# Optimization experiments

Measured on AMD Instinct MI355X. Metric: run time of the kernel, lower is better.

Reference implementation:

```python
import jax, jax.numpy as jnp
import numpy as np


def setup_inputs() -> dict:
    key = jax.random.key(0)
    k1, k2 = jax.random.split(key)
    support_features = jax.random.normal(k1, (1000, 5, 512), dtype=jnp.float32)
    query_features = jax.random.normal(k2, (5000, 512), dtype=jnp.float32)
    return {"support_features": support_features, "query_features": query_features, "use_cosine": 1}


def reference(support_features, query_features, use_cosine):
    # Preprocess: mean-center over (classes, shots), then L2-normalize per vector.
    mean = jnp.mean(support_features, axis=(0, 1), keepdims=True)  # [1,1,D]
    s = support_features - mean                                    # [C,S,D]
    q = query_features - mean[0]                                   # [Q,D]
    s = s / jnp.linalg.norm(s, axis=2, keepdims=True)
    q = q / jnp.linalg.norm(q, axis=1, keepdims=True)
    if use_cosine:
        # cosine sims without materializing [C,Q,S,D]; einsum fuses the dot.
        sims = jnp.einsum('csd,qd->cqs', s, q)   # [C,Q,S]
        best = jnp.max(sims, axis=2)             # [C,Q] best shot per class
        return jnp.argmax(best, axis=0)          # [Q] predicted class
    else:
        # euclidean cdist(query[Q,D], support[C,S,D]) -> [C,Q,S]
        d2 = (jnp.sum(q * q, axis=1)[None, :, None]
              + jnp.sum(s * s, axis=2)[:, None, :]
              - 2.0 * jnp.einsum('csd,qd->cqs', s, q))
        dist = jnp.sqrt(jnp.maximum(d2, 0.0))
        best = jnp.min(dist, axis=2)
        return jnp.argmin(best, axis=0)
```

## Files before the change

kernel.cpp:

```cpp
#include <hip/hip_runtime.h>
#include <stdint.h>

#define D     512
#define NSUP  5000
#define NQRY  5000
#define NPAD  5120
#define MEAN_BLOCKS 100
#define ROWS_PER_MEAN_BLOCK 50
#define SCALE 512.0f

#define OFF_SHI     0
#define OFF_SLO     5242880
#define OFF_QHI     10485760
#define OFF_QLO     15728640
#define OFF_PARTIAL 20971520
#define OFF_MEAN    21176320
#define OFF_KEYS    21178368

typedef _Float16 half4v __attribute__((ext_vector_type(4)));
typedef _Float16 half8v __attribute__((ext_vector_type(8)));
typedef float    f32x4  __attribute__((ext_vector_type(4)));

__device__ __forceinline__ unsigned long long pack_key(float v, int sidx) {
    unsigned u = __float_as_uint(v);
    u = (u & 0x80000000u) ? ~u : (u | 0x80000000u);
    return ((unsigned long long)u << 32) | (unsigned)(0xFFFFFFFFu - (unsigned)sidx);
}

__device__ __forceinline__ void gload16(const void* g, void* l) {
    __builtin_amdgcn_global_load_lds(
        (const __attribute__((address_space(1))) unsigned int*)g,
        (__attribute__((address_space(3))) unsigned int*)l, 16, 0, 0);
}

__global__ void k_partial_mean(const float* __restrict__ sup, float* __restrict__ partial) {
    const int col = threadIdx.x;
    const int b   = blockIdx.x;
    const int r0  = b * ROWS_PER_MEAN_BLOCK;
    float acc = 0.0f;
    for (int r = 0; r < ROWS_PER_MEAN_BLOCK; ++r)
        acc += sup[(size_t)(r0 + r) * D + col];
    partial[b * D + col] = acc;
}

__global__ void k_mean_init(const float* __restrict__ partial, float* __restrict__ mean,
                            unsigned long long* __restrict__ keys) {
    const int col = threadIdx.x;
    float acc = 0.0f;
    for (int b = 0; b < MEAN_BLOCKS; ++b) acc += partial[b * D + col];
    mean[col] = acc * (1.0f / (float)NSUP);
    for (int i = col; i < NSUP; i += 512) keys[i] = 0ull;
}

__global__ void k_split(const float* __restrict__ sup, const float* __restrict__ qry,
                        const float* __restrict__ mean,
                        _Float16* __restrict__ shi, _Float16* __restrict__ slo,
                        _Float16* __restrict__ qhi, _Float16* __restrict__ qlo) {
    const int b = blockIdx.x;
    const int t = threadIdx.x;
    const float* src; _Float16 *dhi, *dlo; int valid;
    if (b < NPAD) { src = sup + (size_t)b * D;
                    dhi = shi + (size_t)b * D; dlo = slo + (size_t)b * D; valid = (b < NSUP); }
    else        { int r = b - NPAD; src = qry + (size_t)r * D;
                    dhi = qhi + (size_t)r * D; dlo = qlo + (size_t)r * D; valid = (r < NQRY); }
    if (!valid) {
        half4v z = {};
        *(half4v*)(dhi + t * 4) = z;
        *(half4v*)(dlo + t * 4) = z;
        return;
    }
    float4 v = *(const float4*)(src + t * 4);
    float4 m = *(const float4*)(mean + t * 4);
    v.x -= m.x; v.y -= m.y; v.z -= m.z; v.w -= m.w;
    float ss = v.x * v.x + v.y * v.y + v.z * v.z + v.w * v.w;
    #pragma unroll
    for (int off = 32; off > 0; off >>= 1) ss += __shfl_down(ss, off, 64);
    __shared__ float red[2];
    if ((t & 63) == 0) red[t >> 6] = ss;
    __syncthreads();
    const float rn = SCALE / sqrtf(red[0] + red[1]);
    float sv[4] = {v.x * rn, v.y * rn, v.z * rn, v.w * rn};
    half4v h, l;
    #pragma unroll
    for (int i = 0; i < 4; ++i) {
        _Float16 hh = (_Float16)sv[i];
        h[i] = hh;
        l[i] = (_Float16)(sv[i] - (float)hh);
    }
    *(half4v*)(dhi + t * 4) = h;
    *(half4v*)(dlo + t * 4) = l;
}

__launch_bounds__(256)
__global__ void k_main(const _Float16* __restrict__ shi, const _Float16* __restrict__ slo,
                       const _Float16* __restrict__ qhi, const _Float16* __restrict__ qlo,
                       unsigned long long* __restrict__ keys) {
    __shared__ __align__(16) _Float16 lds_shi[128 * 32];
    __shared__ __align__(16) _Float16 lds_slo[128 * 32];
    __shared__ __align__(16) _Float16 lds_qhi[128 * 32];
    __shared__ __align__(16) _Float16 lds_qlo[128 * 32];
    __shared__ unsigned long long kl[128];

    const int tid  = threadIdx.x;
    const int lane = tid & 63;
    const int wv   = tid >> 6;
    const int q0   = blockIdx.x * 128;
    const int s0   = blockIdx.y * 128;

    const int m0  = wv * 32 + (lane >> 2);
    const int m1  = m0 + 16;
    const int sl0 = ((lane & 3) ^ ((m0 >> 1) & 3)) * 16;
    const int sl1 = ((lane & 3) ^ ((m1 >> 1) & 3)) * 16;
    const char* pShi = (const char*)shi; const char* pSlo = (const char*)slo;
    const char* pQhi = (const char*)qhi; const char* pQlo = (const char*)qlo;
    const size_t rS0 = (size_t)(s0 + m0) * 1024 + sl0;
    const size_t rS1 = (size_t)(s0 + m1) * 1024 + sl1;
    const size_t rQ0 = (size_t)(q0 + m0) * 1024 + sl0;
    const size_t rQ1 = (size_t)(q0 + m1) * 1024 + sl1;
    _Float16* dj0 = (_Float16*)0;
    _Float16* d_shi0 = lds_shi + wv * 1024;      _Float16* d_shi1 = lds_shi + wv * 1024 + 512;
    _Float16* d_slo0 = lds_slo + wv * 1024;      _Float16* d_slo1 = lds_slo + wv * 1024 + 512;
    _Float16* d_qhi0 = lds_qhi + wv * 1024;      _Float16* d_qhi1 = lds_qhi + wv * 1024 + 512;
    _Float16* d_qlo0 = lds_qlo + wv * 1024;      _Float16* d_qlo1 = lds_qlo + wv * 1024 + 512;
    (void)dj0;

    const int l15 = lane & 15;
    const int kg  = lane >> 4;
    const int fo  = l15 * 64 + ((kg ^ ((l15 >> 1) & 3)) * 16);
    const int sm  = (wv & 1) * 64;
    const int qm  = (wv >> 1) * 64;
    const char* fShi = (const char*)lds_shi + (size_t)sm * 64 + fo;
    const char* fSlo = (const char*)lds_slo + (size_t)sm * 64 + fo;
    const char* fQhi = (const char*)lds_qhi + (size_t)qm * 64 + fo;
    const char* fQlo = (const char*)lds_qlo + (size_t)qm * 64 + fo;

    f32x4 acc[4][4] = {};
    if (tid < 128) kl[tid] = 0ull;

    for (int kc = 0; kc < D; kc += 32) {
        const size_t kb = (size_t)kc * 2;
        __syncthreads();
        gload16(pShi + rS0 + kb, d_shi0);  gload16(pShi + rS1 + kb, d_shi1);
        gload16(pSlo + rS0 + kb, d_slo0);  gload16(pSlo + rS1 + kb, d_slo1);
        gload16(pQhi + rQ0 + kb, d_qhi0);  gload16(pQhi + rQ1 + kb, d_qhi1);
        gload16(pQlo + rQ0 + kb, d_qlo0);  gload16(pQlo + rQ1 + kb, d_qlo1);
        __syncthreads();

        half8v ah[4], al[4], bh[4], bl[4];
        #pragma unroll
        for (int f = 0; f < 4; ++f) {
            ah[f] = *(const half8v*)(fShi + f * 1024);
            al[f] = *(const half8v*)(fSlo + f * 1024);
            bh[f] = *(const half8v*)(fQhi + f * 1024);
            bl[f] = *(const half8v*)(fQlo + f * 1024);
        }
        #pragma unroll
        for (int fa = 0; fa < 4; ++fa)
            #pragma unroll
            for (int fb = 0; fb < 4; ++fb) {
                acc[fa][fb] = __builtin_amdgcn_mfma_f32_16x16x32_f16(ah[fa], bh[fb], acc[fa][fb], 0, 0, 0);
                acc[fa][fb] = __builtin_amdgcn_mfma_f32_16x16x32_f16(ah[fa], bl[fb], acc[fa][fb], 0, 0, 0);
                acc[fa][fb] = __builtin_amdgcn_mfma_f32_16x16x32_f16(al[fa], bh[fb], acc[fa][fb], 0, 0, 0);
            }
    }

    __syncthreads();
    #pragma unroll
    for (int fb = 0; fb < 4; ++fb) {
        unsigned long long best = 0ull;
        #pragma unroll
        for (int fa = 0; fa < 4; ++fa)
            #pragma unroll
            for (int r = 0; r < 4; ++r) {
                const int s = s0 + sm + fa * 16 + kg * 4 + r;
                if (s < NSUP) {
                    unsigned long long k = pack_key(acc[fa][fb][r], s);
                    if (k > best) best = k;
                }
            }
        unsigned long long o = __shfl_xor(best, 16, 64); if (o > best) best = o;
        o = __shfl_xor(best, 32, 64);                    if (o > best) best = o;
        if (kg == 0) atomicMax(&kl[qm + fb * 16 + l15], best);
    }
    __syncthreads();
    if (tid < 128) {
        const int q = q0 + tid;
        if (q < NQRY && kl[tid] != 0ull) atomicMax(&keys[q], kl[tid]);
    }
}

__global__ void k_decode(const unsigned long long* __restrict__ keys, int* __restrict__ out) {
    const int q = blockIdx.x * 256 + threadIdx.x;
    if (q < NQRY) {
        unsigned sidx = 0xFFFFFFFFu - (unsigned)(keys[q] & 0xFFFFFFFFull);
        out[q] = (int)(sidx / 5u);
    }
}

extern "C" void kernel_launch(void* const* d_in, const int* in_sizes, int n_in,
                              void* d_out, int out_size, void* d_ws, size_t ws_size,
                              hipStream_t stream) {
    const float* sup = (const float*)d_in[0];
    const float* qry = (const float*)d_in[1];
    int* out = (int*)d_out;

    char* ws = (char*)d_ws;
    _Float16* shi = (_Float16*)(ws + OFF_SHI);
    _Float16* slo = (_Float16*)(ws + OFF_SLO);
    _Float16* qhi = (_Float16*)(ws + OFF_QHI);
    _Float16* qlo = (_Float16*)(ws + OFF_QLO);
    float* partial = (float*)(ws + OFF_PARTIAL);
    float* mean    = (float*)(ws + OFF_MEAN);
    unsigned long long* keys = (unsigned long long*)(ws + OFF_KEYS);

    k_partial_mean<<<MEAN_BLOCKS, 512, 0, stream>>>(sup, partial);
    k_mean_init<<<1, 512, 0, stream>>>(partial, mean, keys);
    k_split<<<2 * NPAD, 128, 0, stream>>>(sup, qry, mean, shi, slo, qhi, qlo);
    dim3 grid(NPAD / 128, NPAD / 128);
    k_main<<<grid, 256, 0, stream>>>(shi, slo, qhi, qlo, keys);
    k_decode<<<(NQRY + 255) / 256, 256, 0, stream>>>(keys, out);
}
```

Baseline: 179.9 us.

## Double-buffer LDS tiles in the main MFMA loop and pack split rows per block

The main kernel now ping-pongs between two LDS buffers, issuing the async global-to-LDS loads for the next K chunk before computing the current one. This halves the barriers per K step and hides global load latency behind MFMA work. The split kernel now handles four rows per 512-thread block instead of one row per 128-thread block, and the mean loops get unroll pragmas. The cost is doubled LDS use in the main kernel (about 64KB per block), which may reduce how many blocks fit on each CU.

```diff
diff --git a/kernel.cpp b/kernel.cpp
--- a/kernel.cpp
+++ b/kernel.cpp
@@ -38,6 +38,7 @@
     const int b   = blockIdx.x;
     const int r0  = b * ROWS_PER_MEAN_BLOCK;
     float acc = 0.0f;
+    #pragma unroll 5
     for (int r = 0; r < ROWS_PER_MEAN_BLOCK; ++r)
         acc += sup[(size_t)(r0 + r) * D + col];
     partial[b * D + col] = acc;
@@ -47,6 +48,7 @@
                             unsigned long long* __restrict__ keys) {
     const int col = threadIdx.x;
     float acc = 0.0f;
+    #pragma unroll 4
     for (int b = 0; b < MEAN_BLOCKS; ++b) acc += partial[b * D + col];
     mean[col] = acc * (1.0f / (float)NSUP);
     for (int i = col; i < NSUP; i += 512) keys[i] = 0ull;
@@ -56,29 +58,31 @@
                         const float* __restrict__ mean,
                         _Float16* __restrict__ shi, _Float16* __restrict__ slo,
                         _Float16* __restrict__ qhi, _Float16* __restrict__ qlo) {
-    const int b = blockIdx.x;
-    const int t = threadIdx.x;
+    const int t    = threadIdx.x;
+    const int rloc = t >> 7;
+    const int tc   = t & 127;
+    const int b    = (int)blockIdx.x * 4 + rloc;
     const float* src; _Float16 *dhi, *dlo; int valid;
     if (b < NPAD) { src = sup + (size_t)b * D;
                     dhi = shi + (size_t)b * D; dlo = slo + (size_t)b * D; valid = (b < NSUP); }
-    else        { int r = b - NPAD; src = qry + (size_t)r * D;
+    else          { int r = b - NPAD; src = qry + (size_t)r * D;
                     dhi = qhi + (size_t)r * D; dlo = qlo + (size_t)r * D; valid = (r < NQRY); }
+    __shared__ float red[8];
     if (!valid) {
         half4v z = {};
-        *(half4v*)(dhi + t * 4) = z;
-        *(half4v*)(dlo + t * 4) = z;
+        *(half4v*)(dhi + tc * 4) = z;
+        *(half4v*)(dlo + tc * 4) = z;
         return;
     }
-    float4 v = *(const float4*)(src + t * 4);
-    float4 m = *(const float4*)(mean + t * 4);
+    float4 v = *(const float4*)(src + tc * 4);
+    float4 m = *(const float4*)(mean + tc * 4);
     v.x -= m.x; v.y -= m.y; v.z -= m.z; v.w -= m.w;
     float ss = v.x * v.x + v.y * v.y + v.z * v.z + v.w * v.w;
     #pragma unroll
     for (int off = 32; off > 0; off >>= 1) ss += __shfl_down(ss, off, 64);
-    __shared__ float red[2];
     if ((t & 63) == 0) red[t >> 6] = ss;
     __syncthreads();
-    const float rn = SCALE / sqrtf(red[0] + red[1]);
+    const float rn = SCALE / sqrtf(red[rloc * 2] + red[rloc * 2 + 1]);
     float sv[4] = {v.x * rn, v.y * rn, v.z * rn, v.w * rn};
     half4v h, l;
     #pragma unroll
@@ -87,18 +91,18 @@
         h[i] = hh;
         l[i] = (_Float16)(sv[i] - (float)hh);
     }
-    *(half4v*)(dhi + t * 4) = h;
-    *(half4v*)(dlo + t * 4) = l;
+    *(half4v*)(dhi + tc * 4) = h;
+    *(half4v*)(dlo + tc * 4) = l;
 }
 
 __launch_bounds__(256)
 __global__ void k_main(const _Float16* __restrict__ shi, const _Float16* __restrict__ slo,
                        const _Float16* __restrict__ qhi, const _Float16* __restrict__ qlo,
                        unsigned long long* __restrict__ keys) {
-    __shared__ __align__(16) _Float16 lds_shi[128 * 32];
-    __shared__ __align__(16) _Float16 lds_slo[128 * 32];
-    __shared__ __align__(16) _Float16 lds_qhi[128 * 32];
-    __shared__ __align__(16) _Float16 lds_qlo[128 * 32];
+    __shared__ __align__(16) _Float16 lds_shi[2 * 4096];
+    __shared__ __align__(16) _Float16 lds_slo[2 * 4096];
+    __shared__ __align__(16) _Float16 lds_qhi[2 * 4096];
+    __shared__ __align__(16) _Float16 lds_qlo[2 * 4096];
     __shared__ unsigned long long kl[128];
 
     const int tid  = threadIdx.x;
@@ -117,12 +121,10 @@
     const size_t rS1 = (size_t)(s0 + m1) * 1024 + sl1;
     const size_t rQ0 = (size_t)(q0 + m0) * 1024 + sl0;
     const size_t rQ1 = (size_t)(q0 + m1) * 1024 + sl1;
-    _Float16* dj0 = (_Float16*)0;
     _Float16* d_shi0 = lds_shi + wv * 1024;      _Float16* d_shi1 = lds_shi + wv * 1024 + 512;
     _Float16* d_slo0 = lds_slo + wv * 1024;      _Float16* d_slo1 = lds_slo + wv * 1024 + 512;
     _Float16* d_qhi0 = lds_qhi + wv * 1024;      _Float16* d_qhi1 = lds_qhi + wv * 1024 + 512;
     _Float16* d_qlo0 = lds_qlo + wv * 1024;      _Float16* d_qlo1 = lds_qlo + wv * 1024 + 512;
-    (void)dj0;
 
     const int l15 = lane & 15;
     const int kg  = lane >> 4;
@@ -137,34 +139,52 @@
     f32x4 acc[4][4] = {};
     if (tid < 128) kl[tid] = 0ull;
 
-    for (int kc = 0; kc < D; kc += 32) {
-        const size_t kb = (size_t)kc * 2;
+#define STAGE(B, KC) do {                                                          \
+        const size_t kb_ = (size_t)(KC) * 2;                                       \
+        gload16(pShi + rS0 + kb_, d_shi0 + (B) * 4096);                            \
+        gload16(pShi + rS1 + kb_, d_shi1 + (B) * 4096);                            \
+        gload16(pSlo + rS0 + kb_, d_slo0 + (B) * 4096);                            \
+        gload16(pSlo + rS1 + kb_, d_slo1 + (B) * 4096);                            \
+        gload16(pQhi + rQ0 + kb_, d_qhi0 + (B) * 4096);                            \
+        gload16(pQhi + rQ1 + kb_, d_qhi1 + (B) * 4096);                            \
+        gload16(pQlo + rQ0 + kb_, d_qlo0 + (B) * 4096);                            \
+        gload16(pQlo + rQ1 + kb_, d_qlo1 + (B) * 4096);                            \
+    } while (0)
+
+#define COMPUTE(B) do {                                                            \
+        half8v ah[4], al[4], bh[4], bl[4];                                         \
+        _Pragma("unroll")                                                          \
+        for (int f = 0; f < 4; ++f) {                                              \
+            ah[f] = *(const half8v*)(fShi + (B) * 8192 + f * 1024);                \
+            al[f] = *(const half8v*)(fSlo + (B) * 8192 + f * 1024);                \
+            bh[f] = *(const half8v*)(fQhi + (B) * 8192 + f * 1024);                \
+            bl[f] = *(const half8v*)(fQlo + (B) * 8192 + f * 1024);                \
+        }                                                                          \
+        _Pragma("unroll")                                                          \
+        for (int fa = 0; fa < 4; ++fa)                                             \
+            _Pragma("unroll")                                                      \
+            for (int fb = 0; fb < 4; ++fb) {                                       \
+                acc[fa][fb] = __builtin_amdgcn_mfma_f32_16x16x32_f16(ah[fa], bh[fb], acc[fa][fb], 0, 0, 0); \
+                acc[fa][fb] = __builtin_amdgcn_mfma_f32_16x16x32_f16(ah[fa], bl[fb], acc[fa][fb], 0, 0, 0); \
+                acc[fa][fb] = __builtin_amdgcn_mfma_f32_16x16x32_f16(al[fa], bh[fb], acc[fa][fb], 0, 0, 0); \
+            }                                                                      \
+    } while (0)
+
+    STAGE(0, 0);
+    __syncthreads();
+
+    for (int i = 0; i < 8; ++i) {
+        const int kc = i * 64;
+        STAGE(1, kc + 32);
+        COMPUTE(0);
         __syncthreads();
-        gload16(pShi + rS0 + kb, d_shi0);  gload16(pShi + rS1 + kb, d_shi1);
-        gload16(pSlo + rS0 + kb, d_slo0);  gload16(pSlo + rS1 + kb, d_slo1);
-        gload16(pQhi + rQ0 + kb, d_qhi0);  gload16(pQhi + rQ1 + kb, d_qhi1);
-        gload16(pQlo + rQ0 + kb, d_qlo0);  gload16(pQlo + rQ1 + kb, d_qlo1);
+        if (i < 7) STAGE(0, kc + 64);
+        COMPUTE(1);
         __syncthreads();
-
-        half8v ah[4], al[4], bh[4], bl[4];
-        #pragma unroll
-        for (int f = 0; f < 4; ++f) {
-            ah[f] = *(const half8v*)(fShi + f * 1024);
-            al[f] = *(const half8v*)(fSlo + f * 1024);
-            bh[f] = *(const half8v*)(fQhi + f * 1024);
-            bl[f] = *(const half8v*)(fQlo + f * 1024);
-        }
-        #pragma unroll
-        for (int fa = 0; fa < 4; ++fa)
-            #pragma unroll
-            for (int fb = 0; fb < 4; ++fb) {
-                acc[fa][fb] = __builtin_amdgcn_mfma_f32_16x16x32_f16(ah[fa], bh[fb], acc[fa][fb], 0, 0, 0);
-                acc[fa][fb] = __builtin_amdgcn_mfma_f32_16x16x32_f16(ah[fa], bl[fb], acc[fa][fb], 0, 0, 0);
-                acc[fa][fb] = __builtin_amdgcn_mfma_f32_16x16x32_f16(al[fa], bh[fb], acc[fa][fb], 0, 0, 0);
-            }
-    }
-
-    __syncthreads();
+    }
+#undef STAGE
+#undef COMPUTE
+
     #pragma unroll
     for (int fb = 0; fb < 4; ++fb) {
         unsigned long long best = 0ull;
@@ -215,7 +235,7 @@
 
     k_partial_mean<<<MEAN_BLOCKS, 512, 0, stream>>>(sup, partial);
     k_mean_init<<<1, 512, 0, stream>>>(partial, mean, keys);
-    k_split<<<2 * NPAD, 128, 0, stream>>>(sup, qry, mean, shi, slo, qhi, qlo);
+    k_split<<<(2 * NPAD) / 4, 512, 0, stream>>>(sup, qry, mean, shi, slo, qhi, qlo);
     dim3 grid(NPAD / 128, NPAD / 128);
     k_main<<<grid, 256, 0, stream>>>(shi, slo, qhi, qlo, keys);
     k_decode<<<(NQRY + 255) / 256, 256, 0, stream>>>(keys, out);
```

Measured after the change: 184.1 us. +2.3%, slower.
